# Optimization experiments

Measured on AMD Instinct MI355X. Metric: run time of the kernel, lower is better.

Reference implementation:

```python
import jax, jax.numpy as jnp
import numpy as np

B, N, S, K = 8, 16384, 1024, 32
C_STEM, C_PATCH, PE_DIM = 64, 128, 24
RADIUS = 0.2
NUM_BANDS = PE_DIM // 6  # 4 freq bands, sin+cos per xyz axis -> 3*2*4 = 24


def setup_inputs() -> dict:
    key = jax.random.key(0)
    ks = jax.random.split(key, 6)
    xyz = jax.random.uniform(ks[0], (B, N, 3), dtype=jnp.float32)
    point_feature = jax.random.normal(ks[1], (B, N, C_STEM), dtype=jnp.float32)
    patch_center = jax.random.uniform(ks[2], (B, S, 3), dtype=jnp.float32)
    in_dim = C_STEM + 3 + PE_DIM  # grouped_feature + relative_xyz + pos-enc
    w1 = jax.random.normal(ks[3], (in_dim, C_PATCH), dtype=jnp.float32) / np.sqrt(in_dim)
    b1 = jnp.zeros((C_PATCH,), dtype=jnp.float32)
    w2 = jax.random.normal(ks[4], (C_PATCH, C_PATCH), dtype=jnp.float32) / np.sqrt(C_PATCH)
    b2 = jnp.zeros((C_PATCH,), dtype=jnp.float32)
    return dict(xyz=xyz, point_feature=point_feature, patch_center=patch_center,
                w1=w1, b1=b1, w2=w2, b2=b2)


def query_ball_point(radius, nsample, xyz, new_xyz):
    # Standard PointNet++ ball query. xyz:[B,N,3], new_xyz:[B,S,3] -> idx:[B,S,K]
    n = xyz.shape[1]
    sqrdists = jnp.sum((new_xyz[:, :, None, :] - xyz[:, None, :, :]) ** 2, axis=-1)  # [B,S,N]
    gi = jnp.where(sqrdists > radius * radius, n,
                   jnp.arange(n, dtype=jnp.int32)[None, None, :])
    gi = jnp.sort(gi, axis=-1)[:, :, :nsample]           # first K in-ball indices
    first = gi[:, :, :1]
    gi = jnp.where(gi == n, first, gi)                   # pad misses with first hit
    return jnp.minimum(gi, n - 1)


def index_points(points, idx):
    # points:[B,N,C], idx:[B,S,K] -> [B,S,K,C]
    b = points.shape[0]
    return points[jnp.arange(b)[:, None, None], idx]


def pos_encode(rel):
    # NeRF-style sinusoidal encoding of relative xyz: [...,3] -> [...,PE_DIM]
    freqs = (2.0 ** jnp.arange(NUM_BANDS, dtype=jnp.float32)) * jnp.pi
    ang = rel[..., None] * freqs                          # [...,3,NB]
    enc = jnp.concatenate([jnp.sin(ang), jnp.cos(ang)], axis=-1)  # [...,3,2NB]
    return enc.reshape(rel.shape[:-1] + (PE_DIM,))


def reference(xyz, point_feature, patch_center, w1, b1, w2, b2):
    neighbor_idx = query_ball_point(RADIUS, K, xyz, patch_center)   # [B,S,K]
    grouped_xyz = index_points(xyz, neighbor_idx)                    # [B,S,K,3]
    grouped_feature = index_points(point_feature, neighbor_idx)      # [B,S,K,C_STEM]
    relative_xyz = grouped_xyz - patch_center[:, :, None, :]
    relative_position = pos_encode(relative_xyz)                     # [B,S,K,PE_DIM]
    grouped_input = jnp.concatenate(
        (grouped_feature, relative_xyz, relative_position), axis=-1)  # [B,S,K,91]
    h = jax.nn.relu(grouped_input @ w1 + b1)   # PointMLP 1 (shared per-point MLP)
    h = h @ w2 + b2                            # PointMLP 2 (no activation)
    patch_feature = jnp.max(h, axis=2)         # max-pool over K neighbors -> [B,S,C_PATCH]
    return (patch_feature, neighbor_idx)
```

## Files before the change

kernel.cpp:

```cpp
#include <hip/hip_runtime.h>
#include <hip/hip_bf16.h>

#define B_ 8
#define N_ 16384
#define S_ 1024
#define K_ 32
#define CSTEM 64
#define CPATCH 128
#define INDIM 91
#define LDA 104
#define LDH 136
#define NQ 4
#define CHUNK 2048

typedef __attribute__((ext_vector_type(8))) short short8v;
typedef __attribute__((ext_vector_type(4))) float f32x4;

static __device__ __forceinline__ unsigned short f2bf(float f) {
  union { float f; unsigned int u; } v; v.f = f;
  return (unsigned short)((v.u + 0x7FFFu + ((v.u >> 16) & 1u)) >> 16);
}

__global__ __launch_bounds__(256) void pack_weights(
    const float* __restrict__ w1, const float* __restrict__ w2,
    unsigned short* __restrict__ w1p, unsigned short* __restrict__ w2p)
{
  const int id = blockIdx.x * 256 + threadIdx.x;
  if (id < 3 * 8 * 64) {
    const int l = id & 63, ct = (id >> 6) & 7, ks = id >> 9;
    const int col = 16 * ct + (l & 15);
    const int kb = 32 * ks + (l >> 4) * 8;
    unsigned short v[8];
    #pragma unroll
    for (int j = 0; j < 8; ++j) {
      const int k = kb + j;
      v[j] = (k < INDIM) ? f2bf(w1[k * CPATCH + col]) : (unsigned short)0;
    }
    *(short8v*)&w1p[(size_t)id * 8] = *(const short8v*)v;
  } else if (id < 3 * 8 * 64 + 4 * 8 * 64) {
    const int id2 = id - 3 * 8 * 64;
    const int l = id2 & 63, ct = (id2 >> 6) & 7, ks = id2 >> 9;
    const int col = 16 * ct + (l & 15);
    const int kb = 32 * ks + (l >> 4) * 8;
    unsigned short v[8];
    #pragma unroll
    for (int j = 0; j < 8; ++j) v[j] = f2bf(w2[(kb + j) * CPATCH + col]);
    *(short8v*)&w2p[(size_t)id2 * 8] = *(const short8v*)v;
  }
}

__global__ __launch_bounds__(256) void fused_patch(
    const float* __restrict__ xyz, const float* __restrict__ pf,
    const float* __restrict__ pc,
    const unsigned short* __restrict__ w1p, const float* __restrict__ b1,
    const unsigned short* __restrict__ w2p, const float* __restrict__ b2,
    float* __restrict__ idx_out, float* __restrict__ out)
{
  const int tid  = threadIdx.x;
  const int lane = tid & 63;
  const int w    = tid >> 6;
  const int bs0  = blockIdx.x * NQ;
  const int b    = bs0 >> 10;

  __shared__ float scen[3 * NQ];
  __shared__ int   sidx[NQ][K_];
  __shared__ float sxyz[NQ][K_][3];
  __shared__ int   swsum[4][NQ];
  __shared__ int   sfound[NQ];
  __shared__ __align__(16) unsigned short As[NQ * K_][LDA];
  __shared__ __align__(16) unsigned short Hs[K_][LDH];

  const float* __restrict__ xb  = xyz + (size_t)b * N_ * 3;
  const float* __restrict__ pfb = pf  + (size_t)b * N_ * CSTEM;

  if (tid < 3 * NQ) scen[tid] = pc[bs0 * 3 + tid];
  __syncthreads();

  float cxf[NQ], cyf[NQ], czf[NQ];
  #pragma unroll
  for (int q = 0; q < NQ; ++q) {
    cxf[q] = scen[q * 3 + 0];
    cyf[q] = scen[q * 3 + 1];
    czf[q] = scen[q * 3 + 2];
  }
  const double rr = 0.2 * 0.2;

  int found[NQ] = {0, 0, 0, 0};
  const unsigned long long lower = (1ull << lane) - 1ull;

  for (int chunk = 0; chunk < N_; chunk += CHUNK) {
    const int i0 = chunk + tid * 8;
    float px[8], py[8], pz[8];
    {
      const float4 v0 = *(const float4*)&xb[i0 * 3 + 0];
      const float4 v1 = *(const float4*)&xb[i0 * 3 + 4];
      const float4 v2 = *(const float4*)&xb[i0 * 3 + 8];
      const float4 v3 = *(const float4*)&xb[i0 * 3 + 12];
      const float4 v4 = *(const float4*)&xb[i0 * 3 + 16];
      const float4 v5 = *(const float4*)&xb[i0 * 3 + 20];
      px[0] = v0.x; py[0] = v0.y; pz[0] = v0.z;
      px[1] = v0.w; py[1] = v1.x; pz[1] = v1.y;
      px[2] = v1.z; py[2] = v1.w; pz[2] = v2.x;
      px[3] = v2.y; py[3] = v2.z; pz[3] = v2.w;
      px[4] = v3.x; py[4] = v3.y; pz[4] = v3.z;
      px[5] = v3.w; py[5] = v4.x; pz[5] = v4.y;
      px[6] = v4.z; py[6] = v4.w; pz[6] = v5.x;
      px[7] = v5.y; py[7] = v5.z; pz[7] = v5.w;
    }

    unsigned mask[NQ];
    #pragma unroll
    for (int q = 0; q < NQ; ++q) {
      mask[q] = 0u;
      if (found[q] < K_) {
        #pragma unroll
        for (int p = 0; p < 8; ++p) {
          const float dxf = px[p] - cxf[q];
          const float dyf = py[p] - cyf[q];
          const float dzf = pz[p] - czf[q];
          const float d2f = fmaf(dxf, dxf, fmaf(dyf, dyf, dzf * dzf));
          bool in;
          if (fabsf(d2f - 0.04f) <= 1e-5f) {
            const double dx = (double)px[p] - (double)cxf[q];
            const double dy = (double)py[p] - (double)cyf[q];
            const double dz = (double)pz[p] - (double)czf[q];
            in = (dx * dx + dy * dy + dz * dz) <= rr;
          } else {
            in = (d2f < 0.04f);
          }
          if (in) mask[q] |= (1u << p);
        }
      }
    }

    const int c0 = __popc(mask[0]), c1 = __popc(mask[1]);
    const int c2 = __popc(mask[2]), c3 = __popc(mask[3]);
    unsigned pA = (unsigned)c0 | ((unsigned)c1 << 16);
    unsigned pB = (unsigned)c2 | ((unsigned)c3 << 16);
    #pragma unroll
    for (int d = 1; d < 64; d <<= 1) {
      const unsigned vA = (unsigned)__shfl_up((int)pA, d);
      const unsigned vB = (unsigned)__shfl_up((int)pB, d);
      if (lane >= d) { pA += vA; pB += vB; }
    }
    int incl[NQ];
    incl[0] = pA & 0xFFFF; incl[1] = pA >> 16;
    incl[2] = pB & 0xFFFF; incl[3] = pB >> 16;
    if (lane == 63) {
      #pragma unroll
      for (int q = 0; q < NQ; ++q) swsum[w][q] = incl[q];
    }
    __syncthreads();

    int cnt[NQ] = {c0, c1, c2, c3};
    #pragma unroll
    for (int q = 0; q < NQ; ++q) {
      if (found[q] < K_) {
        int pos = found[q] + (incl[q] - cnt[q]);
        #pragma unroll
        for (int v = 0; v < 4; ++v) if (v < w) pos += swsum[v][q];
        #pragma unroll
        for (int p = 0; p < 8; ++p) {
          if (mask[q] & (1u << p)) {
            if (pos < K_) {
              sidx[q][pos] = i0 + p;
              sxyz[q][pos][0] = px[p];
              sxyz[q][pos][1] = py[p];
              sxyz[q][pos][2] = pz[p];
            }
            ++pos;
          }
        }
        found[q] += swsum[0][q] + swsum[1][q] + swsum[2][q] + swsum[3][q];
      }
    }
    __syncthreads();
    if (found[0] >= K_ && found[1] >= K_ && found[2] >= K_ && found[3] >= K_)
      break;
  }

  if (tid == 0) {
    #pragma unroll
    for (int q = 0; q < NQ; ++q) {
      sfound[q] = found[q];
      if (found[q] == 0) {
        sidx[q][0] = N_ - 1;
        sxyz[q][0][0] = xb[(N_ - 1) * 3 + 0];
        sxyz[q][0][1] = xb[(N_ - 1) * 3 + 1];
        sxyz[q][0][2] = xb[(N_ - 1) * 3 + 2];
      }
    }
  }
  __syncthreads();
  if (tid < NQ * K_) {
    const int q = tid >> 5, j = tid & 31;
    const int fq = sfound[q];
    const int v   = (j < fq && fq > 0) ? sidx[q][j]    : sidx[q][0];
    const float x = (j < fq && fq > 0) ? sxyz[q][j][0] : sxyz[q][0][0];
    const float y = (j < fq && fq > 0) ? sxyz[q][j][1] : sxyz[q][0][1];
    const float z = (j < fq && fq > 0) ? sxyz[q][j][2] : sxyz[q][0][2];
    sidx[q][j] = v;
    sxyz[q][j][0] = x; sxyz[q][j][1] = y; sxyz[q][j][2] = z;
    idx_out[(size_t)bs0 * K_ + tid] = (float)v;
  }
  __syncthreads();

  short8v w1f[3][2], w2f[4][2];
  #pragma unroll
  for (int ks = 0; ks < 3; ++ks)
    #pragma unroll
    for (int t = 0; t < 2; ++t)
      w1f[ks][t] = *(const short8v*)&w1p[((size_t)(ks * 8 + 2 * w + t) * 64 + lane) * 8];
  #pragma unroll
  for (int ks = 0; ks < 4; ++ks)
    #pragma unroll
    for (int t = 0; t < 2; ++t)
      w2f[ks][t] = *(const short8v*)&w2p[((size_t)(ks * 8 + 2 * w + t) * 64 + lane) * 8];
  const float bias1[2] = { b1[32 * w + (lane & 15)], b1[32 * w + 16 + (lane & 15)] };
  const float bias2[2] = { b2[32 * w + (lane & 15)], b2[32 * w + 16 + (lane & 15)] };

  {
    const int row = tid >> 3, sub = tid & 7;
    #pragma unroll
    for (int q = 0; q < NQ; ++q) {
      const int r = sidx[q][row];
      const float4 f0 = *(const float4*)&pfb[(size_t)r * CSTEM + sub * 8];
      const float4 f1 = *(const float4*)&pfb[(size_t)r * CSTEM + sub * 8 + 4];
      unsigned short v[8];
      v[0] = f2bf(f0.x); v[1] = f2bf(f0.y); v[2] = f2bf(f0.z); v[3] = f2bf(f0.w);
      v[4] = f2bf(f1.x); v[5] = f2bf(f1.y); v[6] = f2bf(f1.z); v[7] = f2bf(f1.w);
      *(short8v*)&As[q * K_ + row][sub * 8] = *(const short8v*)v;
    }
  }
  {
    const int row = tid & 31, j = tid >> 5;
    #pragma unroll
    for (int q = 0; q < NQ; ++q) {
      const float r0 = sxyz[q][row][0] - cxf[q];
      const float r1 = sxyz[q][row][1] - cyf[q];
      const float r2 = sxyz[q][row][2] - czf[q];
      #pragma unroll
      for (int cc = 0; cc < 4; ++cc) {
        const int c = 64 + 4 * j + cc;
        float val;
        if (c < 67) val = (c == 64) ? r0 : ((c == 65) ? r1 : r2);
        else if (c < 91) {
          const int qq = c - 67, d = qq >> 3, rbit = qq & 7, band = rbit & 3;
          const float rel = (d == 0) ? r0 : ((d == 1) ? r1 : r2);
          const float ang = rel * ((float)(1 << band) * 3.14159265358979323846f);
          val = (rbit < 4) ? __sinf(ang) : __cosf(ang);
        } else val = 0.f;
        As[q * K_ + row][c] = f2bf(val);
      }
    }
  }
  __syncthreads();

  #pragma unroll 1
  for (int q = 0; q < NQ; ++q) {
    f32x4 acc[2][2] = {};
    #pragma unroll
    for (int ks = 0; ks < 3; ++ks) {
      const int k0 = ks * 32 + (lane >> 4) * 8;
      const short8v a0 = *(const short8v*)&As[q * K_ + (lane & 15)][k0];
      const short8v a1 = *(const short8v*)&As[q * K_ + 16 + (lane & 15)][k0];
      acc[0][0] = __builtin_amdgcn_mfma_f32_16x16x32_bf16(a0, w1f[ks][0], acc[0][0], 0, 0, 0);
      acc[0][1] = __builtin_amdgcn_mfma_f32_16x16x32_bf16(a0, w1f[ks][1], acc[0][1], 0, 0, 0);
      acc[1][0] = __builtin_amdgcn_mfma_f32_16x16x32_bf16(a1, w1f[ks][0], acc[1][0], 0, 0, 0);
      acc[1][1] = __builtin_amdgcn_mfma_f32_16x16x32_bf16(a1, w1f[ks][1], acc[1][1], 0, 0, 0);
    }
    #pragma unroll
    for (int rt = 0; rt < 2; ++rt)
      #pragma unroll
      for (int t = 0; t < 2; ++t)
        #pragma unroll
        for (int reg = 0; reg < 4; ++reg) {
          const float h = fmaxf(acc[rt][t][reg] + bias1[t], 0.f);
          const int row = 16 * rt + (lane >> 4) * 4 + reg;
          const int col = 32 * w + 16 * t + (lane & 15);
          Hs[row][col] = f2bf(h);
        }
    __syncthreads();

    f32x4 acc2[2][2] = {};
    #pragma unroll
    for (int ks = 0; ks < 4; ++ks) {
      const int k0 = ks * 32 + (lane >> 4) * 8;
      const short8v a0 = *(const short8v*)&Hs[(lane & 15)][k0];
      const short8v a1 = *(const short8v*)&Hs[16 + (lane & 15)][k0];
      acc2[0][0] = __builtin_amdgcn_mfma_f32_16x16x32_bf16(a0, w2f[ks][0], acc2[0][0], 0, 0, 0);
      acc2[0][1] = __builtin_amdgcn_mfma_f32_16x16x32_bf16(a0, w2f[ks][1], acc2[0][1], 0, 0, 0);
      acc2[1][0] = __builtin_amdgcn_mfma_f32_16x16x32_bf16(a1, w2f[ks][0], acc2[1][0], 0, 0, 0);
      acc2[1][1] = __builtin_amdgcn_mfma_f32_16x16x32_bf16(a1, w2f[ks][1], acc2[1][1], 0, 0, 0);
    }
    float m0 = -3.4e38f, m1 = -3.4e38f;
    #pragma unroll
    for (int rt = 0; rt < 2; ++rt)
      #pragma unroll
      for (int reg = 0; reg < 4; ++reg) {
        m0 = fmaxf(m0, acc2[rt][0][reg]);
        m1 = fmaxf(m1, acc2[rt][1][reg]);
      }
    m0 += bias2[0];
    m1 += bias2[1];
    m0 = fmaxf(m0, __shfl_xor(m0, 16));
    m0 = fmaxf(m0, __shfl_xor(m0, 32));
    m1 = fmaxf(m1, __shfl_xor(m1, 16));
    m1 = fmaxf(m1, __shfl_xor(m1, 32));
    if (lane < 16) {
      out[(size_t)(bs0 + q) * CPATCH + 32 * w + lane]      = m0;
      out[(size_t)(bs0 + q) * CPATCH + 32 * w + 16 + lane] = m1;
    }
    __syncthreads();
  }
}

extern "C" void kernel_launch(void* const* d_in, const int* in_sizes, int n_in,
                              void* d_out, int out_size, void* d_ws, size_t ws_size,
                              hipStream_t stream) {
  const float* xyz = (const float*)d_in[0];
  const float* pf  = (const float*)d_in[1];
  const float* pc  = (const float*)d_in[2];
  const float* w1  = (const float*)d_in[3];
  const float* b1  = (const float*)d_in[4];
  const float* w2  = (const float*)d_in[5];
  const float* b2  = (const float*)d_in[6];

  float* out     = (float*)d_out;
  float* idx_out = out + (size_t)B_ * S_ * CPATCH;

  unsigned short* w1p = (unsigned short*)d_ws;
  unsigned short* w2p = w1p + 96 * 128;

  pack_weights<<<14, 256, 0, stream>>>(w1, w2, w1p, w2p);
  fused_patch<<<B_ * S_ / NQ, 256, 0, stream>>>(xyz, pf, pc, w1p, b1, w2p, b2,
                                                idx_out, out);
}
```

Baseline: 53.60 us.

## Build MLP1 A-fragments in registers and double-buffer hidden tile

Drops the shared-memory As staging tile. Each wave now gathers point features straight from global memory and computes the positional-encoding fragments directly into MFMA operand registers for each query. The hidden-activation buffer is double-buffered, which removes the trailing barrier per query iteration. The trade-off is that every wave redundantly gathers the same neighbor rows and recomputes sin/cos (four times the work across waves), in exchange for lower LDS use and fewer barriers.

```diff
diff --git a/kernel.cpp b/kernel.cpp
--- a/kernel.cpp
+++ b/kernel.cpp
@@ -8,7 +8,6 @@
 #define CSTEM 64
 #define CPATCH 128
 #define INDIM 91
-#define LDA 104
 #define LDH 136
 #define NQ 4
 #define CHUNK 2048
@@ -19,6 +18,36 @@
 static __device__ __forceinline__ unsigned short f2bf(float f) {
   union { float f; unsigned int u; } v; v.f = f;
   return (unsigned short)((v.u + 0x7FFFu + ((v.u >> 16) & 1u)) >> 16);
+}
+
+static __device__ __forceinline__ short8v cvt8(const float4 a, const float4 b) {
+  unsigned short v[8];
+  v[0] = f2bf(a.x); v[1] = f2bf(a.y); v[2] = f2bf(a.z); v[3] = f2bf(a.w);
+  v[4] = f2bf(b.x); v[5] = f2bf(b.y); v[6] = f2bf(b.z); v[7] = f2bf(b.w);
+  return *(const short8v*)v;
+}
+
+static __device__ __forceinline__ short8v pe_frag(
+    float r0, float r1, float r2, int kq)
+{
+  unsigned short v[8];
+  #pragma unroll
+  for (int j = 0; j < 8; ++j) {
+    const int c = 64 + kq + j;
+    float val;
+    if (c < 67) {
+      val = (c == 64) ? r0 : ((c == 65) ? r1 : r2);
+    } else if (c < 91) {
+      const int qq = c - 67, d = qq >> 3, rbit = qq & 7, band = rbit & 3;
+      const float rel = (d == 0) ? r0 : ((d == 1) ? r1 : r2);
+      const float ang = rel * ((float)(1 << band) * 3.14159265358979323846f);
+      val = (rbit < 4) ? __sinf(ang) : __cosf(ang);
+    } else {
+      val = 0.f;
+    }
+    v[j] = f2bf(val);
+  }
+  return *(const short8v*)v;
 }
 
 __global__ __launch_bounds__(256) void pack_weights(
@@ -67,8 +96,7 @@
   __shared__ float sxyz[NQ][K_][3];
   __shared__ int   swsum[4][NQ];
   __shared__ int   sfound[NQ];
-  __shared__ __align__(16) unsigned short As[NQ * K_][LDA];
-  __shared__ __align__(16) unsigned short Hs[K_][LDH];
+  __shared__ __align__(16) unsigned short Hs[2][K_][LDH];
 
   const float* __restrict__ xb  = xyz + (size_t)b * N_ * 3;
   const float* __restrict__ pfb = pf  + (size_t)b * N_ * CSTEM;
@@ -86,7 +114,6 @@
   const double rr = 0.2 * 0.2;
 
   int found[NQ] = {0, 0, 0, 0};
-  const unsigned long long lower = (1ull << lane) - 1ull;
 
   for (int chunk = 0; chunk < N_; chunk += CHUNK) {
     const int i0 = chunk + tid * 8;
@@ -219,56 +246,52 @@
   const float bias1[2] = { b1[32 * w + (lane & 15)], b1[32 * w + 16 + (lane & 15)] };
   const float bias2[2] = { b2[32 * w + (lane & 15)], b2[32 * w + 16 + (lane & 15)] };
 
-  {
-    const int row = tid >> 3, sub = tid & 7;
-    #pragma unroll
-    for (int q = 0; q < NQ; ++q) {
-      const int r = sidx[q][row];
-      const float4 f0 = *(const float4*)&pfb[(size_t)r * CSTEM + sub * 8];
-      const float4 f1 = *(const float4*)&pfb[(size_t)r * CSTEM + sub * 8 + 4];
-      unsigned short v[8];
-      v[0] = f2bf(f0.x); v[1] = f2bf(f0.y); v[2] = f2bf(f0.z); v[3] = f2bf(f0.w);
-      v[4] = f2bf(f1.x); v[5] = f2bf(f1.y); v[6] = f2bf(f1.z); v[7] = f2bf(f1.w);
-      *(short8v*)&As[q * K_ + row][sub * 8] = *(const short8v*)v;
-    }
-  }
-  {
-    const int row = tid & 31, j = tid >> 5;
-    #pragma unroll
-    for (int q = 0; q < NQ; ++q) {
-      const float r0 = sxyz[q][row][0] - cxf[q];
-      const float r1 = sxyz[q][row][1] - cyf[q];
-      const float r2 = sxyz[q][row][2] - czf[q];
-      #pragma unroll
-      for (int cc = 0; cc < 4; ++cc) {
-        const int c = 64 + 4 * j + cc;
-        float val;
-        if (c < 67) val = (c == 64) ? r0 : ((c == 65) ? r1 : r2);
-        else if (c < 91) {
-          const int qq = c - 67, d = qq >> 3, rbit = qq & 7, band = rbit & 3;
-          const float rel = (d == 0) ? r0 : ((d == 1) ? r1 : r2);
-          const float ang = rel * ((float)(1 << band) * 3.14159265358979323846f);
-          val = (rbit < 4) ? __sinf(ang) : __cosf(ang);
-        } else val = 0.f;
-        As[q * K_ + row][c] = f2bf(val);
-      }
-    }
-  }
-  __syncthreads();
+  const int rfr = lane & 15;
+  const int kq  = (lane >> 4) * 8;
 
   #pragma unroll 1
   for (int q = 0; q < NQ; ++q) {
+    const int hb = q & 1;
+    const float cq0 = scen[q * 3 + 0];
+    const float cq1 = scen[q * 3 + 1];
+    const float cq2 = scen[q * 3 + 2];
+
+    const int r0 = sidx[q][rfr];
+    const int r1 = sidx[q][16 + rfr];
+
+    const float4 u00 = *(const float4*)&pfb[(size_t)r0 * CSTEM + kq];
+    const float4 u01 = *(const float4*)&pfb[(size_t)r0 * CSTEM + kq + 4];
+    const float4 u02 = *(const float4*)&pfb[(size_t)r0 * CSTEM + 32 + kq];
+    const float4 u03 = *(const float4*)&pfb[(size_t)r0 * CSTEM + 32 + kq + 4];
+    const float4 u10 = *(const float4*)&pfb[(size_t)r1 * CSTEM + kq];
+    const float4 u11 = *(const float4*)&pfb[(size_t)r1 * CSTEM + kq + 4];
+    const float4 u12 = *(const float4*)&pfb[(size_t)r1 * CSTEM + 32 + kq];
+    const float4 u13 = *(const float4*)&pfb[(size_t)r1 * CSTEM + 32 + kq + 4];
+
+    const short8v a0k2 = pe_frag(sxyz[q][rfr][0] - cq0,
+                                 sxyz[q][rfr][1] - cq1,
+                                 sxyz[q][rfr][2] - cq2, kq);
+    const short8v a1k2 = pe_frag(sxyz[q][16 + rfr][0] - cq0,
+                                 sxyz[q][16 + rfr][1] - cq1,
+                                 sxyz[q][16 + rfr][2] - cq2, kq);
+
+    const short8v a0k0 = cvt8(u00, u01), a0k1 = cvt8(u02, u03);
+    const short8v a1k0 = cvt8(u10, u11), a1k1 = cvt8(u12, u13);
+
     f32x4 acc[2][2] = {};
-    #pragma unroll
-    for (int ks = 0; ks < 3; ++ks) {
-      const int k0 = ks * 32 + (lane >> 4) * 8;
-      const short8v a0 = *(const short8v*)&As[q * K_ + (lane & 15)][k0];
-      const short8v a1 = *(const short8v*)&As[q * K_ + 16 + (lane & 15)][k0];
-      acc[0][0] = __builtin_amdgcn_mfma_f32_16x16x32_bf16(a0, w1f[ks][0], acc[0][0], 0, 0, 0);
-      acc[0][1] = __builtin_amdgcn_mfma_f32_16x16x32_bf16(a0, w1f[ks][1], acc[0][1], 0, 0, 0);
-      acc[1][0] = __builtin_amdgcn_mfma_f32_16x16x32_bf16(a1, w1f[ks][0], acc[1][0], 0, 0, 0);
-      acc[1][1] = __builtin_amdgcn_mfma_f32_16x16x32_bf16(a1, w1f[ks][1], acc[1][1], 0, 0, 0);
-    }
+    acc[0][0] = __builtin_amdgcn_mfma_f32_16x16x32_bf16(a0k0, w1f[0][0], acc[0][0], 0, 0, 0);
+    acc[0][1] = __builtin_amdgcn_mfma_f32_16x16x32_bf16(a0k0, w1f[0][1], acc[0][1], 0, 0, 0);
+    acc[1][0] = __builtin_amdgcn_mfma_f32_16x16x32_bf16(a1k0, w1f[0][0], acc[1][0], 0, 0, 0);
+    acc[1][1] = __builtin_amdgcn_mfma_f32_16x16x32_bf16(a1k0, w1f[0][1], acc[1][1], 0, 0, 0);
+    acc[0][0] = __builtin_amdgcn_mfma_f32_16x16x32_bf16(a0k1, w1f[1][0], acc[0][0], 0, 0, 0);
+    acc[0][1] = __builtin_amdgcn_mfma_f32_16x16x32_bf16(a0k1, w1f[1][1], acc[0][1], 0, 0, 0);
+    acc[1][0] = __builtin_amdgcn_mfma_f32_16x16x32_bf16(a1k1, w1f[1][0], acc[1][0], 0, 0, 0);
+    acc[1][1] = __builtin_amdgcn_mfma_f32_16x16x32_bf16(a1k1, w1f[1][1], acc[1][1], 0, 0, 0);
+    acc[0][0] = __builtin_amdgcn_mfma_f32_16x16x32_bf16(a0k2, w1f[2][0], acc[0][0], 0, 0, 0);
+    acc[0][1] = __builtin_amdgcn_mfma_f32_16x16x32_bf16(a0k2, w1f[2][1], acc[0][1], 0, 0, 0);
+    acc[1][0] = __builtin_amdgcn_mfma_f32_16x16x32_bf16(a1k2, w1f[2][0], acc[1][0], 0, 0, 0);
+    acc[1][1] = __builtin_amdgcn_mfma_f32_16x16x32_bf16(a1k2, w1f[2][1], acc[1][1], 0, 0, 0);
+
     #pragma unroll
     for (int rt = 0; rt < 2; ++rt)
       #pragma unroll
@@ -278,16 +301,16 @@
           const float h = fmaxf(acc[rt][t][reg] + bias1[t], 0.f);
           const int row = 16 * rt + (lane >> 4) * 4 + reg;
           const int col = 32 * w + 16 * t + (lane & 15);
-          Hs[row][col] = f2bf(h);
+          Hs[hb][row][col] = f2bf(h);
         }
     __syncthreads();
 
     f32x4 acc2[2][2] = {};
     #pragma unroll
     for (int ks = 0; ks < 4; ++ks) {
-      const int k0 = ks * 32 + (lane >> 4) * 8;
-      const short8v a0 = *(const short8v*)&Hs[(lane & 15)][k0];
-      const short8v a1 = *(const short8v*)&Hs[16 + (lane & 15)][k0];
+      const int k0 = ks * 32 + kq;
+      const short8v a0 = *(const short8v*)&Hs[hb][rfr][k0];
+      const short8v a1 = *(const short8v*)&Hs[hb][16 + rfr][k0];
       acc2[0][0] = __builtin_amdgcn_mfma_f32_16x16x32_bf16(a0, w2f[ks][0], acc2[0][0], 0, 0, 0);
       acc2[0][1] = __builtin_amdgcn_mfma_f32_16x16x32_bf16(a0, w2f[ks][1], acc2[0][1], 0, 0, 0);
       acc2[1][0] = __builtin_amdgcn_mfma_f32_16x16x32_bf16(a1, w2f[ks][0], acc2[1][0], 0, 0, 0);
@@ -311,7 +334,6 @@
       out[(size_t)(bs0 + q) * CPATCH + 32 * w + lane]      = m0;
       out[(size_t)(bs0 + q) * CPATCH + 32 * w + 16 + lane] = m1;
     }
-    __syncthreads();
   }
 }
 
```

Result: slower. 67.89 us (+26.7%).

## Assign one wavefront per query in ball search, removing block-wide barriers

Applied to the files above, without the earlier changes.

Restructures the ball query so each of the four wavefronts handles one patch center independently, scanning 1024 points per iteration (16 per lane) with a wave-local prefix scan and its own early exit. This drops the per-chunk __syncthreads and shared-memory cross-wave sums. The cost is that each wave now reads the full xyz stream for its own query, so global or L2 traffic for xyz is up to four times higher, and the block still waits for the slowest wave.

```diff
diff --git a/kernel.cpp b/kernel.cpp
--- a/kernel.cpp
+++ b/kernel.cpp
@@ -11,7 +11,6 @@
 #define LDA 104
 #define LDH 136
 #define NQ 4
-#define CHUNK 2048
 
 typedef __attribute__((ext_vector_type(8))) short short8v;
 typedef __attribute__((ext_vector_type(4))) float f32x4;
@@ -48,6 +47,10 @@
     *(short8v*)&w2p[(size_t)id2 * 8] = *(const short8v*)v;
   }
 }
+
+#define FCOMP(V, IDX) (((IDX) & 3) == 0 ? (V)[(IDX) >> 2].x : \
+                       ((IDX) & 3) == 1 ? (V)[(IDX) >> 2].y : \
+                       ((IDX) & 3) == 2 ? (V)[(IDX) >> 2].z : (V)[(IDX) >> 2].w)
 
 __global__ __launch_bounds__(256) void fused_patch(
     const float* __restrict__ xyz, const float* __restrict__ pf,
@@ -65,7 +68,6 @@
   __shared__ float scen[3 * NQ];
   __shared__ int   sidx[NQ][K_];
   __shared__ float sxyz[NQ][K_][3];
-  __shared__ int   swsum[4][NQ];
   __shared__ int   sfound[NQ];
   __shared__ __align__(16) unsigned short As[NQ * K_][LDA];
   __shared__ __align__(16) unsigned short Hs[K_][LDH];
@@ -76,120 +78,75 @@
   if (tid < 3 * NQ) scen[tid] = pc[bs0 * 3 + tid];
   __syncthreads();
 
-  float cxf[NQ], cyf[NQ], czf[NQ];
-  #pragma unroll
-  for (int q = 0; q < NQ; ++q) {
-    cxf[q] = scen[q * 3 + 0];
-    cyf[q] = scen[q * 3 + 1];
-    czf[q] = scen[q * 3 + 2];
-  }
-  const double rr = 0.2 * 0.2;
-
-  int found[NQ] = {0, 0, 0, 0};
-  const unsigned long long lower = (1ull << lane) - 1ull;
-
-  for (int chunk = 0; chunk < N_; chunk += CHUNK) {
-    const int i0 = chunk + tid * 8;
-    float px[8], py[8], pz[8];
-    {
-      const float4 v0 = *(const float4*)&xb[i0 * 3 + 0];
-      const float4 v1 = *(const float4*)&xb[i0 * 3 + 4];
-      const float4 v2 = *(const float4*)&xb[i0 * 3 + 8];
-      const float4 v3 = *(const float4*)&xb[i0 * 3 + 12];
-      const float4 v4 = *(const float4*)&xb[i0 * 3 + 16];
-      const float4 v5 = *(const float4*)&xb[i0 * 3 + 20];
-      px[0] = v0.x; py[0] = v0.y; pz[0] = v0.z;
-      px[1] = v0.w; py[1] = v1.x; pz[1] = v1.y;
-      px[2] = v1.z; py[2] = v1.w; pz[2] = v2.x;
-      px[3] = v2.y; py[3] = v2.z; pz[3] = v2.w;
-      px[4] = v3.x; py[4] = v3.y; pz[4] = v3.z;
-      px[5] = v3.w; py[5] = v4.x; pz[5] = v4.y;
-      px[6] = v4.z; py[6] = v4.w; pz[6] = v5.x;
-      px[7] = v5.y; py[7] = v5.z; pz[7] = v5.w;
-    }
-
-    unsigned mask[NQ];
-    #pragma unroll
-    for (int q = 0; q < NQ; ++q) {
-      mask[q] = 0u;
-      if (found[q] < K_) {
-        #pragma unroll
-        for (int p = 0; p < 8; ++p) {
-          const float dxf = px[p] - cxf[q];
-          const float dyf = py[p] - cyf[q];
-          const float dzf = pz[p] - czf[q];
-          const float d2f = fmaf(dxf, dxf, fmaf(dyf, dyf, dzf * dzf));
-          bool in;
-          if (fabsf(d2f - 0.04f) <= 1e-5f) {
-            const double dx = (double)px[p] - (double)cxf[q];
-            const double dy = (double)py[p] - (double)cyf[q];
-            const double dz = (double)pz[p] - (double)czf[q];
-            in = (dx * dx + dy * dy + dz * dz) <= rr;
-          } else {
-            in = (d2f < 0.04f);
+  {
+    const int q = w;
+    const float cx = scen[q * 3 + 0];
+    const float cy = scen[q * 3 + 1];
+    const float cz = scen[q * 3 + 2];
+    const double rr = 0.2 * 0.2;
+
+    int found = 0;
+    for (int base = 0; base < N_; base += 1024) {
+      const int i0 = base + lane * 16;
+      float4 v[12];
+      #pragma unroll
+      for (int t = 0; t < 12; ++t)
+        v[t] = *(const float4*)&xb[i0 * 3 + t * 4];
+
+      unsigned mask = 0u;
+      #pragma unroll
+      for (int p = 0; p < 16; ++p) {
+        const float X = FCOMP(v, 3 * p + 0);
+        const float Y = FCOMP(v, 3 * p + 1);
+        const float Z = FCOMP(v, 3 * p + 2);
+        const float dxf = X - cx, dyf = Y - cy, dzf = Z - cz;
+        const float d2f = fmaf(dxf, dxf, fmaf(dyf, dyf, dzf * dzf));
+        bool in;
+        if (fabsf(d2f - 0.04f) <= 1e-5f) {
+          const double dx = (double)X - (double)cx;
+          const double dy = (double)Y - (double)cy;
+          const double dz = (double)Z - (double)cz;
+          in = (dx * dx + dy * dy + dz * dz) <= rr;
+        } else {
+          in = (d2f < 0.04f);
+        }
+        if (in) mask |= (1u << p);
+      }
+
+      const int cnt = __popc(mask);
+      int incl = cnt;
+      #pragma unroll
+      for (int d = 1; d < 64; d <<= 1) {
+        const int t = __shfl_up(incl, d);
+        if (lane >= d) incl += t;
+      }
+      const int tot = __shfl(incl, 63);
+
+      int pos = found + (incl - cnt);
+      #pragma unroll
+      for (int p = 0; p < 16; ++p) {
+        if (mask & (1u << p)) {
+          if (pos < K_) {
+            sidx[q][pos] = i0 + p;
+            sxyz[q][pos][0] = FCOMP(v, 3 * p + 0);
+            sxyz[q][pos][1] = FCOMP(v, 3 * p + 1);
+            sxyz[q][pos][2] = FCOMP(v, 3 * p + 2);
           }
-          if (in) mask[q] |= (1u << p);
+          ++pos;
         }
       }
-    }
-
-    const int c0 = __popc(mask[0]), c1 = __popc(mask[1]);
-    const int c2 = __popc(mask[2]), c3 = __popc(mask[3]);
-    unsigned pA = (unsigned)c0 | ((unsigned)c1 << 16);
-    unsigned pB = (unsigned)c2 | ((unsigned)c3 << 16);
-    #pragma unroll
-    for (int d = 1; d < 64; d <<= 1) {
-      const unsigned vA = (unsigned)__shfl_up((int)pA, d);
-      const unsigned vB = (unsigned)__shfl_up((int)pB, d);
-      if (lane >= d) { pA += vA; pB += vB; }
-    }
-    int incl[NQ];
-    incl[0] = pA & 0xFFFF; incl[1] = pA >> 16;
-    incl[2] = pB & 0xFFFF; incl[3] = pB >> 16;
-    if (lane == 63) {
-      #pragma unroll
-      for (int q = 0; q < NQ; ++q) swsum[w][q] = incl[q];
-    }
-    __syncthreads();
-
-    int cnt[NQ] = {c0, c1, c2, c3};
-    #pragma unroll
-    for (int q = 0; q < NQ; ++q) {
-      if (found[q] < K_) {
-        int pos = found[q] + (incl[q] - cnt[q]);
-        #pragma unroll
-        for (int v = 0; v < 4; ++v) if (v < w) pos += swsum[v][q];
-        #pragma unroll
-        for (int p = 0; p < 8; ++p) {
-          if (mask[q] & (1u << p)) {
-            if (pos < K_) {
-              sidx[q][pos] = i0 + p;
-              sxyz[q][pos][0] = px[p];
-              sxyz[q][pos][1] = py[p];
-              sxyz[q][pos][2] = pz[p];
-            }
-            ++pos;
-          }
-        }
-        found[q] += swsum[0][q] + swsum[1][q] + swsum[2][q] + swsum[3][q];
-      }
-    }
-    __syncthreads();
-    if (found[0] >= K_ && found[1] >= K_ && found[2] >= K_ && found[3] >= K_)
-      break;
-  }
-
-  if (tid == 0) {
-    #pragma unroll
-    for (int q = 0; q < NQ; ++q) {
-      sfound[q] = found[q];
-      if (found[q] == 0) {
-        sidx[q][0] = N_ - 1;
-        sxyz[q][0][0] = xb[(N_ - 1) * 3 + 0];
-        sxyz[q][0][1] = xb[(N_ - 1) * 3 + 1];
-        sxyz[q][0][2] = xb[(N_ - 1) * 3 + 2];
-      }
-    }
+      found += tot;
+      if (found >= K_) break;
+    }
+    if (lane == 0) sfound[q] = found;
+  }
+  __syncthreads();
+
+  if (tid < NQ && sfound[tid] == 0) {
+    sidx[tid][0] = N_ - 1;
+    sxyz[tid][0][0] = xb[(N_ - 1) * 3 + 0];
+    sxyz[tid][0][1] = xb[(N_ - 1) * 3 + 1];
+    sxyz[tid][0][2] = xb[(N_ - 1) * 3 + 2];
   }
   __syncthreads();
   if (tid < NQ * K_) {
@@ -226,19 +183,19 @@
       const int r = sidx[q][row];
       const float4 f0 = *(const float4*)&pfb[(size_t)r * CSTEM + sub * 8];
       const float4 f1 = *(const float4*)&pfb[(size_t)r * CSTEM + sub * 8 + 4];
-      unsigned short v[8];
-      v[0] = f2bf(f0.x); v[1] = f2bf(f0.y); v[2] = f2bf(f0.z); v[3] = f2bf(f0.w);
-      v[4] = f2bf(f1.x); v[5] = f2bf(f1.y); v[6] = f2bf(f1.z); v[7] = f2bf(f1.w);
-      *(short8v*)&As[q * K_ + row][sub * 8] = *(const short8v*)v;
+      unsigned short vv[8];
+      vv[0] = f2bf(f0.x); vv[1] = f2bf(f0.y); vv[2] = f2bf(f0.z); vv[3] = f2bf(f0.w);
+      vv[4] = f2bf(f1.x); vv[5] = f2bf(f1.y); vv[6] = f2bf(f1.z); vv[7] = f2bf(f1.w);
+      *(short8v*)&As[q * K_ + row][sub * 8] = *(const short8v*)vv;
     }
   }
   {
     const int row = tid & 31, j = tid >> 5;
     #pragma unroll
     for (int q = 0; q < NQ; ++q) {
-      const float r0 = sxyz[q][row][0] - cxf[q];
-      const float r1 = sxyz[q][row][1] - cyf[q];
-      const float r2 = sxyz[q][row][2] - czf[q];
+      const float r0 = sxyz[q][row][0] - scen[q * 3 + 0];
+      const float r1 = sxyz[q][row][1] - scen[q * 3 + 1];
+      const float r2 = sxyz[q][row][2] - scen[q * 3 + 2];
       #pragma unroll
       for (int cc = 0; cc < 4; ++cc) {
         const int c = 64 + 4 * j + cc;
```

Result: faster. 50.22 us (-6.3%).
